# Kernel tuning notes

Measured on AMD Instinct MI355X. Metric: run time of the kernel, lower is better.

Reference implementation:

```python
import jax, jax.numpy as jnp
import numpy as np

N = 100000          # nodes
E = 3200000         # edges (avg degree 32)
F_IN = 128
HID = [128, 256, 128, 64, 32]
EPS = 1e-5


def setup_inputs() -> dict:
    key = jax.random.key(0)
    ks = jax.random.split(key, 64)
    inp = {}
    inp["x"] = jax.random.normal(ks[0], (N, F_IN), dtype=jnp.float32)
    inp["edge_index"] = jax.random.randint(ks[1], (2, E), 0, N, dtype=jnp.int64)
    dims = [F_IN] + HID
    k = 2
    for i in range(len(HID)):
        fan_in = dims[i]
        inp[f"W{i}"] = jax.random.normal(ks[k], (dims[i], dims[i + 1]), dtype=jnp.float32) / np.sqrt(fan_in); k += 1
        inp[f"b{i}"] = jnp.zeros((dims[i + 1],), dtype=jnp.float32)
        inp[f"g{i}"] = jnp.ones((dims[i + 1],), dtype=jnp.float32)
        inp[f"be{i}"] = jnp.zeros((dims[i + 1],), dtype=jnp.float32)
    inp["fc_w"] = jax.random.normal(ks[k], (HID[-1], 1), dtype=jnp.float32) / np.sqrt(HID[-1])
    inp["fc_b"] = jnp.zeros((1,), dtype=jnp.float32)
    return inp


def _gcn_forward(x, edge_index, Ws, bs, gs, bes, fc_w, fc_b):
    src, dst = edge_index[0], edge_index[1]
    # symmetric-normalized adjacency with self-loops (PyG GCNConv default,
    # edge_weight=None -> all-ones). deg = in-degree + 1 (self-loop).
    deg = jax.ops.segment_sum(jnp.ones((E,), x.dtype), dst, num_segments=N) + 1.0
    dis = jax.lax.rsqrt(deg)                 # deg^{-1/2}
    di = 1.0 / deg                           # self-loop norm deg^{-1}
    norm = (dis[src] * dis[dst])[:, None]    # [E,1]
    for W, b, g, be in zip(Ws, bs, gs, bes):
        h = x @ W                                                        # [N,d']
        x = jax.ops.segment_sum(norm * h[src], dst, num_segments=N)
        x = x + di[:, None] * h + b                                      # conv out
        mu = jnp.mean(x, axis=0)
        var = jnp.mean(jnp.square(x - mu), axis=0)
        x = (x - mu) * jax.lax.rsqrt(var + EPS) * g + be                 # BatchNorm1d
        x = jax.nn.relu(x)                                               # dropout = eval identity
    edge_emb = x[src] * x[dst]                                           # [E, 32]
    return jax.nn.sigmoid(edge_emb @ fc_w + fc_b)                        # [E, 1]


def reference(x, edge_index, W0, b0, g0, be0, W1, b1, g1, be1, W2, b2, g2, be2,
              W3, b3, g3, be3, W4, b4, g4, be4, fc_w, fc_b):
    Ws = [W0, W1, W2, W3, W4]
    bs = [b0, b1, b2, b3, b4]
    gs = [g0, g1, g2, g3, g4]
    bes = [be0, be1, be2, be3, be4]
    return _gcn_forward(x, edge_index, Ws, bs, gs, bes, fc_w, fc_b)
```

## Files before the change

### kernel.cpp

```cpp
#include <hip/hip_runtime.h>
#include <hip/hip_fp16.h>
#include <cstddef>

#define NN 100000
#define EE 3200000
#define EPSB 1e-5f
#define NB 391
#define BCAP 10240
#define BNBLK 512

typedef _Float16 half8 __attribute__((ext_vector_type(8)));
typedef float floatx4 __attribute__((ext_vector_type(4)));


__global__ __launch_bounds__(256) void k_bscat(const int* __restrict__ src,
                                               const int* __restrict__ dst,
                                               int* __restrict__ bcur,
                                               unsigned* __restrict__ barr) {
    __shared__ int hist[NB];
    __shared__ int base[NB];
    int tid = threadIdx.x;
    for (int b = tid; b < NB; b += 256) hist[b] = 0;
    __syncthreads();
    int e0 = blockIdx.x * 4096;
    int d[16], s[16];
    #pragma unroll
    for (int j = 0; j < 16; j++) {
        int e = e0 + j * 256 + tid;
        if (e < EE) {
            d[j] = dst[e];
            s[j] = src[e];
            atomicAdd(&hist[d[j] >> 8], 1);
        } else d[j] = -1;
    }
    __syncthreads();
    for (int b = tid; b < NB; b += 256) {
        int c = hist[b];
        base[b] = (c > 0) ? atomicAdd(&bcur[b], c) : 0;
        hist[b] = 0;
    }
    __syncthreads();
    #pragma unroll
    for (int j = 0; j < 16; j++) {
        if (d[j] >= 0) {
            int b = d[j] >> 8;
            int r = atomicAdd(&hist[b], 1);
            barr[(size_t)b * BCAP + base[b] + r] =
                (unsigned)s[j] | ((unsigned)(d[j] & 255) << 17);
        }
    }
}

__global__ __launch_bounds__(1024) void k_bdeg(const int* __restrict__ bcur,
                                               const unsigned* __restrict__ barr,
                                               int* __restrict__ degcnt,
                                               float* __restrict__ dis) {
    __shared__ int h[256];
    int b = blockIdx.x;
    if (threadIdx.x < 256) h[threadIdx.x] = 0;
    __syncthreads();
    int cnt = bcur[b];
    const unsigned* p = barr + (size_t)b * BCAP;
    for (int t = threadIdx.x; t < cnt; t += 1024)
        atomicAdd(&h[(p[t] >> 17) & 255], 1);
    __syncthreads();
    if (threadIdx.x < 256) {
        int node = (b << 8) + threadIdx.x;
        if (node < NN) {
            int dg = h[threadIdx.x];
            degcnt[node] = dg;
            dis[node] = rsqrtf((float)dg + 1.0f);
        }
    }
}

__global__ __launch_bounds__(1024) void k_place(const int* __restrict__ bcur,
                                                const unsigned* __restrict__ barr,
                                                const int* __restrict__ rowptr,
                                                int* __restrict__ col) {
    __shared__ int cur[256];
    int b = blockIdx.x;
    if (threadIdx.x < 256) {
        int node = (b << 8) + threadIdx.x;
        cur[threadIdx.x] = (node < NN) ? rowptr[node] : 0;
    }
    __syncthreads();
    int cnt = bcur[b];
    const unsigned* p = barr + (size_t)b * BCAP;
    for (int t = threadIdx.x; t < cnt; t += 1024) {
        unsigned e = p[t];
        int pos = atomicAdd(&cur[(e >> 17) & 255], 1);
        col[pos] = (int)(e & 0x1FFFFu);
    }
}

__global__ void k_scan_block(const int* __restrict__ in, int* __restrict__ out,
                             int* __restrict__ blksum, int n) {
    __shared__ int s[1024];
    int i = blockIdx.x * 1024 + threadIdx.x;
    int v = (i < n) ? in[i] : 0;
    s[threadIdx.x] = v;
    __syncthreads();
    for (int off = 1; off < 1024; off <<= 1) {
        int t = (threadIdx.x >= off) ? s[threadIdx.x - off] : 0;
        __syncthreads();
        s[threadIdx.x] += t;
        __syncthreads();
    }
    if (i < n) out[i] = s[threadIdx.x] - v;
    if (threadIdx.x == 1023) blksum[blockIdx.x] = s[1023];
}

__global__ void k_scan_top(int* __restrict__ blksum, int nb) {
    if (threadIdx.x == 0) {
        int acc = 0;
        for (int b = 0; b < nb; b++) { int v = blksum[b]; blksum[b] = acc; acc += v; }
    }
}

__global__ void k_scan_add(int* __restrict__ out, const int* __restrict__ blksum, int n) {
    int i = blockIdx.x * 1024 + threadIdx.x;
    if (i < n) out[i] += blksum[blockIdx.x];
}


__global__ void k_f2h(const float4* __restrict__ in, uint2* __restrict__ out, int n4) {
    int t = blockIdx.x * blockDim.x + threadIdx.x;
    if (t >= n4) return;
    float4 v = in[t];
    union { __half2 h; unsigned u; } a, b;
    a.h = __floats2half2_rn(v.x, v.y);
    b.h = __floats2half2_rn(v.z, v.w);
    out[t] = make_uint2(a.u, b.u);
}

__global__ void k_wpack_all(const float* __restrict__ W0, const float* __restrict__ W1,
                            const float* __restrict__ W2, const float* __restrict__ W3,
                            const float* __restrict__ W4, __half* __restrict__ Wp) {
    const int offs[6] = {0, 16384, 49152, 81920, 90112, 92160};
    const int Ks[5] = {128, 128, 256, 128, 64};
    const int Ns[5] = {128, 256, 128, 64, 32};
    const float* Ws[5] = {W0, W1, W2, W3, W4};
    int t = blockIdx.x * blockDim.x + threadIdx.x;
    if (t >= 92160) return;
    int l = 0;
    while (t >= offs[l + 1]) l++;
    int local = t - offs[l];
    int N = Ns[l], K = Ks[l];
    int k = local / N, n = local - k * N;
    Wp[(size_t)offs[l] + (size_t)n * K + k] = __float2half(Ws[l][local]);
}


template<int NT, bool OUT16, bool ABN>
__global__ __launch_bounds__(256) void k_mgemm(const void* __restrict__ Av,
                                               const __half* __restrict__ Wp,
                                               void* __restrict__ Cv,
                                               int M, int K, int N,
                                               const float* __restrict__ dis,
                                               const float* __restrict__ bias,
                                               const float* __restrict__ AB) {
    constexpr int TN = NT * 16;
    __shared__ __half Ash[128][40];
    __shared__ __half Bsh[TN][40];
    int tid  = threadIdx.x;
    int wave = tid >> 6;
    int lane = tid & 63;
    int quad = lane >> 4;
    int l16  = lane & 15;
    int bm = blockIdx.x * 128;
    int bn = blockIdx.y * TN;

    floatx4 acc[2][NT];
    #pragma unroll
    for (int mt = 0; mt < 2; mt++)
        #pragma unroll
        for (int nt = 0; nt < NT; nt++)
            acc[mt][nt] = (floatx4){0.f, 0.f, 0.f, 0.f};

    for (int k0 = 0; k0 < K; k0 += 32) {
        #pragma unroll
        for (int it = 0; it < 2; it++) {
            int u = tid + it * 256;
            int row = u >> 2, seg = u & 3;
            int grow = bm + row;
            if (ABN) {
                const float* Af = (const float*)Av;
                int f0 = k0 + seg * 8;
                uint4 o = make_uint4(0, 0, 0, 0);
                if (grow < M) {
                    float4 x0 = *(const float4*)&Af[(size_t)grow * K + f0];
                    float4 x1 = *(const float4*)&Af[(size_t)grow * K + f0 + 4];
                    float4 a0 = *(const float4*)&AB[f0];
                    float4 a1 = *(const float4*)&AB[f0 + 4];
                    float4 c0 = *(const float4*)&AB[K + f0];
                    float4 c1 = *(const float4*)&AB[K + f0 + 4];
                    float h0 = fmaxf(x0.x * a0.x + c0.x, 0.f);
                    float h1 = fmaxf(x0.y * a0.y + c0.y, 0.f);
                    float h2 = fmaxf(x0.z * a0.z + c0.z, 0.f);
                    float h3 = fmaxf(x0.w * a0.w + c0.w, 0.f);
                    float h4 = fmaxf(x1.x * a1.x + c1.x, 0.f);
                    float h5 = fmaxf(x1.y * a1.y + c1.y, 0.f);
                    float h6 = fmaxf(x1.z * a1.z + c1.z, 0.f);
                    float h7 = fmaxf(x1.w * a1.w + c1.w, 0.f);
                    union { __half2 h; unsigned u; } p0, p1, p2, p3;
                    p0.h = __floats2half2_rn(h0, h1);
                    p1.h = __floats2half2_rn(h2, h3);
                    p2.h = __floats2half2_rn(h4, h5);
                    p3.h = __floats2half2_rn(h6, h7);
                    o = make_uint4(p0.u, p1.u, p2.u, p3.u);
                }
                *(uint4*)&Ash[row][seg * 8] = o;
            } else {
                const __half* A = (const __half*)Av;
                uint4 v = make_uint4(0, 0, 0, 0);
                if (grow < M) v = *(const uint4*)&A[(size_t)grow * K + k0 + seg * 8];
                *(uint4*)&Ash[row][seg * 8] = v;
            }
        }
        if (tid < TN * 4) {
            int n = tid >> 2, seg = tid & 3;
            uint4 v = *(const uint4*)&Wp[(size_t)(bn + n) * K + k0 + seg * 8];
            *(uint4*)&Bsh[n][seg * 8] = v;
        }
        __syncthreads();
        half8 a[2], b[NT];
        #pragma unroll
        for (int mt = 0; mt < 2; mt++)
            a[mt] = *(const half8*)&Ash[wave * 32 + mt * 16 + l16][quad * 8];
        #pragma unroll
        for (int nt = 0; nt < NT; nt++)
            b[nt] = *(const half8*)&Bsh[nt * 16 + l16][quad * 8];
        #pragma unroll
        for (int mt = 0; mt < 2; mt++)
            #pragma unroll
            for (int nt = 0; nt < NT; nt++)
                acc[mt][nt] = __builtin_amdgcn_mfma_f32_16x16x32_f16(
                    a[mt], b[nt], acc[mt][nt], 0, 0, 0);
        __syncthreads();
    }

    #pragma unroll
    for (int mt = 0; mt < 2; mt++) {
        #pragma unroll
        for (int r = 0; r < 4; r++) {
            int grow = bm + wave * 32 + mt * 16 + quad * 4 + r;
            if (grow >= M) continue;
            if (OUT16) {
                float ds = dis[grow];
                __half* C = (__half*)Cv;
                #pragma unroll
                for (int nt = 0; nt < NT; nt++) {
                    int gcol = bn + nt * 16 + l16;
                    C[(size_t)grow * N + gcol] = __float2half(ds * acc[mt][nt][r]);
                }
            } else {
                float* C = (float*)Cv;
                #pragma unroll
                for (int nt = 0; nt < NT; nt++) {
                    int gcol = bn + nt * 16 + l16;
                    C[(size_t)grow * N + gcol] = acc[mt][nt][r] + bias[gcol];
                }
            }
        }
    }
}

__global__ void k_nscale(const float* __restrict__ X, const float* __restrict__ AB,
                         const float* __restrict__ dis, uint4* __restrict__ out) {
    int t = blockIdx.x * blockDim.x + threadIdx.x;
    if (t >= NN * 16) return;
    int row = t >> 4;
    int f0 = (t & 15) * 8;
    float ds = dis[row];
    float4 x0 = *(const float4*)&X[(size_t)row * 128 + f0];
    float4 x1 = *(const float4*)&X[(size_t)row * 128 + f0 + 4];
    float4 a0 = *(const float4*)&AB[f0];
    float4 a1 = *(const float4*)&AB[f0 + 4];
    float4 c0 = *(const float4*)&AB[128 + f0];
    float4 c1 = *(const float4*)&AB[128 + f0 + 4];
    float h0 = ds * fmaxf(x0.x * a0.x + c0.x, 0.f);
    float h1 = ds * fmaxf(x0.y * a0.y + c0.y, 0.f);
    float h2 = ds * fmaxf(x0.z * a0.z + c0.z, 0.f);
    float h3 = ds * fmaxf(x0.w * a0.w + c0.w, 0.f);
    float h4 = ds * fmaxf(x1.x * a1.x + c1.x, 0.f);
    float h5 = ds * fmaxf(x1.y * a1.y + c1.y, 0.f);
    float h6 = ds * fmaxf(x1.z * a1.z + c1.z, 0.f);
    float h7 = ds * fmaxf(x1.w * a1.w + c1.w, 0.f);
    union { __half2 h; unsigned u; } p0, p1, p2, p3;
    p0.h = __floats2half2_rn(h0, h1);
    p1.h = __floats2half2_rn(h2, h3);
    p2.h = __floats2half2_rn(h4, h5);
    p3.h = __floats2half2_rn(h6, h7);
    out[t] = make_uint4(p0.u, p1.u, p2.u, p3.u);
}


__device__ __forceinline__ void acc_row(float* acc, const uint4& r) {
    const __half2* hp = (const __half2*)&r;
    #pragma unroll
    for (int k = 0; k < 4; k++) {
        float2 f2 = __half22float2(hp[k]);
        acc[2 * k]     += f2.x;
        acc[2 * k + 1] += f2.y;
    }
}

template<int TPN, bool OUT16>
__global__ __launch_bounds__(256) void k_agg_h(const uint4* __restrict__ Hs,
                                               void* __restrict__ outv,
                                               const int* __restrict__ rowptr,
                                               const int* __restrict__ degcnt,
                                               const int* __restrict__ colv,
                                               const float* __restrict__ dis,
                                               const float* __restrict__ bias) {
    constexpr int G = 256 / TPN;
    int g    = threadIdx.x / TPN;
    int lane = threadIdx.x % TPN;
    int i = blockIdx.x * G + g;
    if (i >= NN) return;
    int beg = rowptr[i];
    int cnt = degcnt[i];
    const uint4* base = Hs + lane;
    float acc[8] = {};
    int e = 0;
    for (; e + 8 <= cnt; e += 8) {
        int c[8];
        #pragma unroll
        for (int j = 0; j < 8; j++) c[j] = colv[beg + e + j];
        uint4 r[8];
        #pragma unroll
        for (int j = 0; j < 8; j++) r[j] = base[(size_t)c[j] * TPN];
        #pragma unroll
        for (int j = 0; j < 8; j++) acc_row(acc, r[j]);
    }
    for (; e < cnt; e++) {
        uint4 r = base[(size_t)colv[beg + e] * TPN];
        acc_row(acc, r);
    }
    uint4 rs = base[(size_t)i * TPN];
    acc_row(acc, rs);
    float ds = dis[i];
    float o[8];
    #pragma unroll
    for (int k = 0; k < 8; k++) o[k] = ds * acc[k];
    if (OUT16) {
        uint4 ov;
        __half2* op = (__half2*)&ov;
        #pragma unroll
        for (int k = 0; k < 4; k++) op[k] = __floats2half2_rn(o[2 * k], o[2 * k + 1]);
        ((uint4*)outv)[(size_t)i * TPN + lane] = ov;
    } else {
        float4 b0 = ((const float4*)bias)[lane * 2];
        float4 b1 = ((const float4*)bias)[lane * 2 + 1];
        o[0] += b0.x; o[1] += b0.y; o[2] += b0.z; o[3] += b0.w;
        o[4] += b1.x; o[5] += b1.y; o[6] += b1.z; o[7] += b1.w;
        float4* out = (float4*)outv;
        size_t ob = (size_t)i * (2 * TPN) + lane * 2;
        out[ob]     = make_float4(o[0], o[1], o[2], o[3]);
        out[ob + 1] = make_float4(o[4], o[5], o[6], o[7]);
    }
}


template<int D>
__global__ __launch_bounds__(256) void k_bnpart(const float4* __restrict__ X4,
                                                float* __restrict__ partial) {
    constexpr int Q   = D / 4;
    constexpr int RPI = 256 / Q;
    int tq = threadIdx.x % Q;
    int rg = threadIdx.x / Q;
    int chunk = (NN + BNBLK - 1) / BNBLK;
    int r0 = blockIdx.x * chunk;
    int r1 = r0 + chunk; if (r1 > NN) r1 = NN;
    float4 s  = {0.f, 0.f, 0.f, 0.f};
    float4 s2 = {0.f, 0.f, 0.f, 0.f};
    for (int r = r0 + rg; r < r1; r += RPI) {
        float4 v = X4[(size_t)r * Q + tq];
        s.x += v.x; s.y += v.y; s.z += v.z; s.w += v.w;
        s2.x += v.x * v.x; s2.y += v.y * v.y; s2.z += v.z * v.z; s2.w += v.w * v.w;
    }
    __shared__ float4 ls[256], ls2[256];
    ls[threadIdx.x] = s; ls2[threadIdx.x] = s2;
    __syncthreads();
    if (threadIdx.x < Q) {
        float4 a = ls[threadIdx.x], b = ls2[threadIdx.x];
        #pragma unroll
        for (int g = 1; g < RPI; g++) {
            float4 u = ls[g * Q + threadIdx.x], w = ls2[g * Q + threadIdx.x];
            a.x += u.x; a.y += u.y; a.z += u.z; a.w += u.w;
            b.x += w.x; b.y += w.y; b.z += w.z; b.w += w.w;
        }
        *(float4*)&partial[(size_t)blockIdx.x * 2 * D + threadIdx.x * 4]     = a;
        *(float4*)&partial[(size_t)blockIdx.x * 2 * D + D + threadIdx.x * 4] = b;
    }
}

template<int D>
__global__ __launch_bounds__(1024) void k_bnfin2(const float* __restrict__ partial,
                                                 const float* __restrict__ g,
                                                 const float* __restrict__ be,
                                                 float* __restrict__ AB) {
    constexpr int G = 1024 / D;
    int f  = threadIdx.x % D;
    int gr = threadIdx.x / D;
    float sum = 0.f, sq = 0.f;
    for (int b = gr; b < BNBLK; b += G) {
        sum += partial[(size_t)b * 2 * D + f];
        sq  += partial[(size_t)b * 2 * D + D + f];
    }
    __shared__ float ls[1024], ls2[1024];
    ls[threadIdx.x] = sum; ls2[threadIdx.x] = sq;
    __syncthreads();
    if (threadIdx.x < D) {
        float a = ls[threadIdx.x], b = ls2[threadIdx.x];
        for (int k = 1; k < G; k++) {
            a += ls[k * D + threadIdx.x];
            b += ls2[k * D + threadIdx.x];
        }
        float mu  = a / (float)NN;
        float var = b / (float)NN - mu * mu;
        var = fmaxf(var, 0.f);
        float inv = rsqrtf(var + EPSB);
        float sc = g[threadIdx.x] * inv;
        AB[threadIdx.x]     = sc;
        AB[D + threadIdx.x] = be[threadIdx.x] - mu * sc;
    }
}

__global__ void k_norm16(const float4* __restrict__ X, const float* __restrict__ AB,
                         uint2* __restrict__ Y, int d, int total4) {
    int t = blockIdx.x * blockDim.x + threadIdx.x;
    if (t >= total4) return;
    int f0 = (t * 4) & (d - 1);
    float4 v = X[t];
    float a0 = AB[f0],     a1 = AB[f0 + 1], a2 = AB[f0 + 2], a3 = AB[f0 + 3];
    float c0 = AB[d + f0], c1 = AB[d + f0 + 1], c2 = AB[d + f0 + 2], c3 = AB[d + f0 + 3];
    float o0 = fmaxf(v.x * a0 + c0, 0.f);
    float o1 = fmaxf(v.y * a1 + c1, 0.f);
    float o2 = fmaxf(v.z * a2 + c2, 0.f);
    float o3 = fmaxf(v.w * a3 + c3, 0.f);
    union { __half2 h; unsigned u; } p, q;
    p.h = __floats2half2_rn(o0, o1);
    q.h = __floats2half2_rn(o2, o3);
    Y[t] = make_uint2(p.u, q.u);
}


__global__ __launch_bounds__(256) void k_edge16(const uint4* __restrict__ X,
                                                const int* __restrict__ src,
                                                const int* __restrict__ dst,
                                                const float* __restrict__ fcw,
                                                const float* __restrict__ fcb,
                                                float* __restrict__ out) {
    int lane = threadIdx.x & 3;
    size_t t = (size_t)blockIdx.x * 256 + threadIdx.x;
    int eid = (int)(t >> 2);
    if (eid >= EE) return;
    int s = src[eid], d = dst[eid];
    uint4 av = X[(size_t)s * 4 + lane];
    uint4 bv = X[(size_t)d * 4 + lane];
    const __half2* ap = (const __half2*)&av;
    const __half2* bp2 = (const __half2*)&bv;
    float v = 0.f;
    #pragma unroll
    for (int k = 0; k < 4; k++) {
        float2 fa = __half22float2(ap[k]);
        float2 fb = __half22float2(bp2[k]);
        float w0 = fcw[lane * 8 + 2 * k];
        float w1 = fcw[lane * 8 + 2 * k + 1];
        v += fa.x * fb.x * w0 + fa.y * fb.y * w1;
    }
    v += __shfl_xor(v, 1, 4);
    v += __shfl_xor(v, 2, 4);
    if (lane == 0) out[eid] = 1.f / (1.f + expf(-(v + fcb[0])));
}


extern "C" void kernel_launch(void* const* d_in, const int* in_sizes, int n_in,
                              void* d_out, int out_size, void* d_ws, size_t ws_size,
                              hipStream_t stream) {
    const float* x0 = (const float*)d_in[0];
    const int* ei   = (const int*)d_in[1];
    const int* srcv = ei;
    const int* dstv = ei + EE;
    const float *W[5], *bp[5], *gp[5], *bep[5];
    int idx = 2;
    for (int l = 0; l < 5; l++) {
        W[l]   = (const float*)d_in[idx++];
        bp[l]  = (const float*)d_in[idx++];
        gp[l]  = (const float*)d_in[idx++];
        bep[l] = (const float*)d_in[idx++];
    }
    const float* fcw = (const float*)d_in[22];
    const float* fcb = (const float*)d_in[23];

    char* ws = (char*)d_ws;
    size_t off = 0;
    auto alloc = [&](size_t bytes) -> void* {
        void* p = ws + off;
        off = (off + bytes + 255) & ~(size_t)255;
        return p;
    };
    float*    bufA    = (float*)   alloc((size_t)NN * 256 * 4);
    __half*   act16   = (__half*)  alloc((size_t)NN * 256 * 2);
    __half*   x16     = (__half*)  alloc((size_t)NN * 128 * 2);
    __half*   Hh      = (__half*)  alloc((size_t)NN * 128 * 2);
    unsigned* barr    = (unsigned*)alloc((size_t)NB * BCAP * 4);
    int*      colv    = (int*)     alloc((size_t)EE * 4);
    int*      rowptr  = (int*)     alloc((size_t)NN * 4);
    int*      degcnt  = (int*)     alloc((size_t)NN * 4);
    float*    dis     = (float*)   alloc((size_t)NN * 4);
    int*      bcur    = (int*)     alloc((size_t)NB * 4);
    int*      scnblk  = (int*)     alloc(4096);
    float*    bnpart  = (float*)   alloc((size_t)BNBLK * 512 * 4);
    float*    bnAB    = (float*)   alloc(512 * 4);
    __half*   Wp      = (__half*)  alloc((size_t)92160 * 2);
    const int woff[5] = {0, 16384, 49152, 81920, 90112};

    hipMemsetAsync(bcur, 0, (size_t)NB * 4, stream);
    k_bscat<<<(EE + 4095) / 4096, 256, 0, stream>>>(srcv, dstv, bcur, barr);
    k_bdeg<<<NB, 1024, 0, stream>>>(bcur, barr, degcnt, dis);
    int nScanBlk = (NN + 1023) / 1024;
    k_scan_block<<<nScanBlk, 1024, 0, stream>>>(degcnt, rowptr, scnblk, NN);
    k_scan_top<<<1, 64, 0, stream>>>(scnblk, nScanBlk);
    k_scan_add<<<nScanBlk, 1024, 0, stream>>>(rowptr, scnblk, NN);
    k_place<<<NB, 1024, 0, stream>>>(bcur, barr, rowptr, colv);

    k_f2h<<<(NN * 128 / 4 + 255) / 256, 256, 0, stream>>>(
        (const float4*)x0, (uint2*)x16, NN * 128 / 4);
    k_wpack_all<<<(92160 + 255) / 256, 256, 0, stream>>>(W[0], W[1], W[2], W[3], W[4], Wp);

    int gx = (NN + 127) / 128;

    {
        dim3 grid(gx, 128 / 64);
        k_mgemm<4, true, false><<<grid, 256, 0, stream>>>(x16, Wp + woff[0], Hh, NN, 128, 128, dis, nullptr, nullptr);
        k_agg_h<16, false><<<(NN + 15) / 16, 256, 0, stream>>>(
            (const uint4*)Hh, bufA, rowptr, degcnt, colv, dis, bp[0]);
        k_bnpart<128><<<BNBLK, 256, 0, stream>>>((const float4*)bufA, bnpart);
        k_bnfin2<128><<<1, 1024, 0, stream>>>(bnpart, gp[0], bep[0], bnAB);
        k_nscale<<<(NN * 16 + 255) / 256, 256, 0, stream>>>(bufA, bnAB, dis, (uint4*)Hh);
    }
    {
        k_agg_h<16, true><<<(NN + 15) / 16, 256, 0, stream>>>(
            (const uint4*)Hh, act16, rowptr, degcnt, colv, dis, nullptr);
        dim3 grid(gx, 256 / 64);
        k_mgemm<4, false, false><<<grid, 256, 0, stream>>>(act16, Wp + woff[1], bufA, NN, 128, 256, nullptr, bp[1], nullptr);
        k_bnpart<256><<<BNBLK, 256, 0, stream>>>((const float4*)bufA, bnpart);
        k_bnfin2<256><<<1, 1024, 0, stream>>>(bnpart, gp[1], bep[1], bnAB);
    }
    {
        dim3 grid(gx, 128 / 64);
        k_mgemm<4, true, true><<<grid, 256, 0, stream>>>(bufA, Wp + woff[2], Hh, NN, 256, 128, dis, nullptr, bnAB);
        k_agg_h<16, false><<<(NN + 15) / 16, 256, 0, stream>>>(
            (const uint4*)Hh, bufA, rowptr, degcnt, colv, dis, bp[2]);
        k_bnpart<128><<<BNBLK, 256, 0, stream>>>((const float4*)bufA, bnpart);
        k_bnfin2<128><<<1, 1024, 0, stream>>>(bnpart, gp[2], bep[2], bnAB);
    }
    {
        dim3 grid(gx, 64 / 64);
        k_mgemm<4, true, true><<<grid, 256, 0, stream>>>(bufA, Wp + woff[3], Hh, NN, 128, 64, dis, nullptr, bnAB);
        k_agg_h<8, false><<<(NN + 31) / 32, 256, 0, stream>>>(
            (const uint4*)Hh, bufA, rowptr, degcnt, colv, dis, bp[3]);
        k_bnpart<64><<<BNBLK, 256, 0, stream>>>((const float4*)bufA, bnpart);
        k_bnfin2<64><<<1, 1024, 0, stream>>>(bnpart, gp[3], bep[3], bnAB);
    }
    {
        dim3 grid(gx, 1);
        k_mgemm<2, true, true><<<grid, 256, 0, stream>>>(bufA, Wp + woff[4], Hh, NN, 64, 32, dis, nullptr, bnAB);
        k_agg_h<4, false><<<(NN + 63) / 64, 256, 0, stream>>>(
            (const uint4*)Hh, bufA, rowptr, degcnt, colv, dis, bp[4]);
        k_bnpart<32><<<BNBLK, 256, 0, stream>>>((const float4*)bufA, bnpart);
        k_bnfin2<32><<<1, 1024, 0, stream>>>(bnpart, gp[4], bep[4], bnAB);
        int total4 = NN * 32 / 4;
        k_norm16<<<(total4 + 255) / 256, 256, 0, stream>>>(
            (const float4*)bufA, bnAB, (uint2*)act16, 32, total4);
    }

    size_t edgeThreads = (size_t)EE * 4;
    k_edge16<<<(unsigned)((edgeThreads + 255) / 256), 256, 0, stream>>>(
        (const uint4*)act16, srcv, dstv, fcw, fcb, (float*)d_out);
}
```

Before: 1.004 ms.

## Quantize gathered features to int8 with per-group scales for first two aggregations

Adds int8 quantization of the node feature rows gathered in the first two layers' aggregations. Layer 0 uses signed values with a zero point and one scale per 8 features; layer 1 uses unsigned values with one scale per 16 features after ReLU. This halves the bytes per gathered row and reuses the edge-bucket buffer for storage. It also deepens the unroll of the fp16 gather loop to 16, with a 4-wide tail. The cost is extra quantize passes, scale-array reads and lower numerical precision.

```diff
diff --git a/kernel.cpp b/kernel.cpp
--- a/kernel.cpp
+++ b/kernel.cpp
@@ -266,8 +266,38 @@
     }
 }
 
-__global__ void k_nscale(const float* __restrict__ X, const float* __restrict__ AB,
-                         const float* __restrict__ dis, uint4* __restrict__ out) {
+
+__global__ __launch_bounds__(256) void k_q8p8(const uint4* __restrict__ H,
+                                              uint2* __restrict__ q8,
+                                              float* __restrict__ scq, int total) {
+    int t = blockIdx.x * 256 + threadIdx.x;
+    if (t >= total) return;
+    uint4 v = H[t];
+    const __half2* hp = (const __half2*)&v;
+    float h[8];
+    #pragma unroll
+    for (int k = 0; k < 4; k++) {
+        float2 f = __half22float2(hp[k]);
+        h[2 * k] = f.x; h[2 * k + 1] = f.y;
+    }
+    float m = fabsf(h[0]);
+    #pragma unroll
+    for (int k = 1; k < 8; k++) m = fmaxf(m, fabsf(h[k]));
+    float inv = m > 0.f ? 127.f / m : 0.f;
+    unsigned b[8];
+    #pragma unroll
+    for (int k = 0; k < 8; k++) {
+        float f = fminf(fmaxf(h[k] * inv, -127.f), 127.f);
+        b[k] = (unsigned)(f + 128.5f);
+    }
+    q8[t] = make_uint2(b[0] | (b[1] << 8) | (b[2] << 16) | (b[3] << 24),
+                       b[4] | (b[5] << 8) | (b[6] << 16) | (b[7] << 24));
+    scq[t] = m * (1.f / 127.f);
+}
+
+__global__ void k_nscale_q8(const float* __restrict__ X, const float* __restrict__ AB,
+                            const float* __restrict__ dis, uint2* __restrict__ q8,
+                            float* __restrict__ scq) {
     int t = blockIdx.x * blockDim.x + threadIdx.x;
     if (t >= NN * 16) return;
     int row = t >> 4;
@@ -279,22 +309,172 @@
     float4 a1 = *(const float4*)&AB[f0 + 4];
     float4 c0 = *(const float4*)&AB[128 + f0];
     float4 c1 = *(const float4*)&AB[128 + f0 + 4];
-    float h0 = ds * fmaxf(x0.x * a0.x + c0.x, 0.f);
-    float h1 = ds * fmaxf(x0.y * a0.y + c0.y, 0.f);
-    float h2 = ds * fmaxf(x0.z * a0.z + c0.z, 0.f);
-    float h3 = ds * fmaxf(x0.w * a0.w + c0.w, 0.f);
-    float h4 = ds * fmaxf(x1.x * a1.x + c1.x, 0.f);
-    float h5 = ds * fmaxf(x1.y * a1.y + c1.y, 0.f);
-    float h6 = ds * fmaxf(x1.z * a1.z + c1.z, 0.f);
-    float h7 = ds * fmaxf(x1.w * a1.w + c1.w, 0.f);
-    union { __half2 h; unsigned u; } p0, p1, p2, p3;
-    p0.h = __floats2half2_rn(h0, h1);
-    p1.h = __floats2half2_rn(h2, h3);
-    p2.h = __floats2half2_rn(h4, h5);
-    p3.h = __floats2half2_rn(h6, h7);
-    out[t] = make_uint4(p0.u, p1.u, p2.u, p3.u);
-}
-
+    float h[8];
+    h[0] = ds * fmaxf(x0.x * a0.x + c0.x, 0.f);
+    h[1] = ds * fmaxf(x0.y * a0.y + c0.y, 0.f);
+    h[2] = ds * fmaxf(x0.z * a0.z + c0.z, 0.f);
+    h[3] = ds * fmaxf(x0.w * a0.w + c0.w, 0.f);
+    h[4] = ds * fmaxf(x1.x * a1.x + c1.x, 0.f);
+    h[5] = ds * fmaxf(x1.y * a1.y + c1.y, 0.f);
+    h[6] = ds * fmaxf(x1.z * a1.z + c1.z, 0.f);
+    h[7] = ds * fmaxf(x1.w * a1.w + c1.w, 0.f);
+    float m = h[0];
+    #pragma unroll
+    for (int k = 1; k < 8; k++) m = fmaxf(m, h[k]);
+    m = fmaxf(m, __shfl_xor(m, 1));
+    float inv = m > 0.f ? 255.f / m : 0.f;
+    unsigned b[8];
+    #pragma unroll
+    for (int k = 0; k < 8; k++)
+        b[k] = (unsigned)(fminf(h[k] * inv, 255.f) + 0.5f);
+    q8[t] = make_uint2(b[0] | (b[1] << 8) | (b[2] << 16) | (b[3] << 24),
+                       b[4] | (b[5] << 8) | (b[6] << 16) | (b[7] << 24));
+    if ((t & 1) == 0) scq[t >> 1] = m * (1.f / 255.f);
+}
+
+
+__device__ __forceinline__ void acc_q8s2(float* acc, const uint4& r,
+                                         const float2& s, float& c0, float& c1) {
+    const unsigned* w = (const unsigned*)&r;
+    c0 += s.x; c1 += s.y;
+    #pragma unroll
+    for (int q = 0; q < 4; q++) {
+        unsigned v = w[q];
+        float sq = (q < 2) ? s.x : s.y;
+        acc[4 * q + 0] = fmaf(sq, (float)(v & 0xffu), acc[4 * q + 0]);
+        acc[4 * q + 1] = fmaf(sq, (float)((v >> 8) & 0xffu), acc[4 * q + 1]);
+        acc[4 * q + 2] = fmaf(sq, (float)((v >> 16) & 0xffu), acc[4 * q + 2]);
+        acc[4 * q + 3] = fmaf(sq, (float)(v >> 24), acc[4 * q + 3]);
+    }
+}
+
+template<int TPN>
+__global__ __launch_bounds__(256) void k_agg_q8s(const uint4* __restrict__ Q,
+                                                 const float* __restrict__ sc,
+                                                 float* __restrict__ outf,
+                                                 const int* __restrict__ rowptr,
+                                                 const int* __restrict__ degcnt,
+                                                 const int* __restrict__ colv,
+                                                 const float* __restrict__ dis,
+                                                 const float* __restrict__ bias) {
+    constexpr int G = 256 / TPN;
+    int g    = threadIdx.x / TPN;
+    int lane = threadIdx.x % TPN;
+    int i = blockIdx.x * G + g;
+    if (i >= NN) return;
+    int beg = rowptr[i];
+    int cnt = degcnt[i];
+    const uint4*  base = Q + lane;
+    const float2* scb  = (const float2*)sc + lane;
+    float acc[16] = {};
+    float c0 = 0.f, c1 = 0.f;
+    int e = 0;
+    for (; e + 8 <= cnt; e += 8) {
+        int c[8];
+        #pragma unroll
+        for (int j = 0; j < 8; j++) c[j] = colv[beg + e + j];
+        uint4 r[8];
+        float2 s[8];
+        #pragma unroll
+        for (int j = 0; j < 8; j++) {
+            r[j] = base[(size_t)c[j] * TPN];
+            s[j] = scb[(size_t)c[j] * TPN];
+        }
+        #pragma unroll
+        for (int j = 0; j < 8; j++) acc_q8s2(acc, r[j], s[j], c0, c1);
+    }
+    for (; e < cnt; e++) {
+        int c = colv[beg + e];
+        uint4 r = base[(size_t)c * TPN];
+        acc_q8s2(acc, r, scb[(size_t)c * TPN], c0, c1);
+    }
+    uint4 rs = base[(size_t)i * TPN];
+    acc_q8s2(acc, rs, scb[(size_t)i * TPN], c0, c1);
+    float ds = dis[i];
+    float zp0 = 128.f * c0, zp1 = 128.f * c1;
+    float o[16];
+    #pragma unroll
+    for (int k = 0; k < 16; k++) o[k] = ds * (acc[k] - (k < 8 ? zp0 : zp1));
+    float4* out = (float4*)outf;
+    const float4* bi = (const float4*)bias;
+    size_t ob = (size_t)i * (4 * TPN) + lane * 4;
+    #pragma unroll
+    for (int j = 0; j < 4; j++) {
+        float4 b = bi[lane * 4 + j];
+        out[ob + j] = make_float4(o[4 * j] + b.x, o[4 * j + 1] + b.y,
+                                  o[4 * j + 2] + b.z, o[4 * j + 3] + b.w);
+    }
+}
+
+__device__ __forceinline__ void acc_q8u(float* acc, const uint4& r, float s) {
+    const unsigned* w = (const unsigned*)&r;
+    #pragma unroll
+    for (int q = 0; q < 4; q++) {
+        unsigned v = w[q];
+        acc[4 * q + 0] = fmaf(s, (float)(v & 0xffu), acc[4 * q + 0]);
+        acc[4 * q + 1] = fmaf(s, (float)((v >> 8) & 0xffu), acc[4 * q + 1]);
+        acc[4 * q + 2] = fmaf(s, (float)((v >> 16) & 0xffu), acc[4 * q + 2]);
+        acc[4 * q + 3] = fmaf(s, (float)(v >> 24), acc[4 * q + 3]);
+    }
+}
+
+template<int TPN>
+__global__ __launch_bounds__(256) void k_agg_q8u(const uint4* __restrict__ Q,
+                                                 const float* __restrict__ sc,
+                                                 __half* __restrict__ out16,
+                                                 const int* __restrict__ rowptr,
+                                                 const int* __restrict__ degcnt,
+                                                 const int* __restrict__ colv,
+                                                 const float* __restrict__ dis) {
+    constexpr int G = 256 / TPN;
+    int g    = threadIdx.x / TPN;
+    int lane = threadIdx.x % TPN;
+    int i = blockIdx.x * G + g;
+    if (i >= NN) return;
+    int beg = rowptr[i];
+    int cnt = degcnt[i];
+    const uint4* base = Q + lane;
+    const float* scb  = sc + lane;
+    float acc[16] = {};
+    int e = 0;
+    for (; e + 8 <= cnt; e += 8) {
+        int c[8];
+        #pragma unroll
+        for (int j = 0; j < 8; j++) c[j] = colv[beg + e + j];
+        uint4 r[8];
+        float s[8];
+        #pragma unroll
+        for (int j = 0; j < 8; j++) {
+            r[j] = base[(size_t)c[j] * TPN];
+            s[j] = scb[(size_t)c[j] * TPN];
+        }
+        #pragma unroll
+        for (int j = 0; j < 8; j++) acc_q8u(acc, r[j], s[j]);
+    }
+    for (; e < cnt; e++) {
+        int c = colv[beg + e];
+        uint4 r = base[(size_t)c * TPN];
+        acc_q8u(acc, r, scb[(size_t)c * TPN]);
+    }
+    uint4 rs = base[(size_t)i * TPN];
+    acc_q8u(acc, rs, scb[(size_t)i * TPN]);
+    float ds = dis[i];
+    float o[16];
+    #pragma unroll
+    for (int k = 0; k < 16; k++) o[k] = ds * acc[k];
+    uint4 ov0, ov1;
+    __half2* p0 = (__half2*)&ov0;
+    __half2* p1 = (__half2*)&ov1;
+    #pragma unroll
+    for (int k = 0; k < 4; k++) {
+        p0[k] = __floats2half2_rn(o[2 * k], o[2 * k + 1]);
+        p1[k] = __floats2half2_rn(o[8 + 2 * k], o[9 + 2 * k]);
+    }
+    uint4* out = (uint4*)out16;
+    size_t ob = (size_t)i * (2 * TPN) + lane * 2;
+    out[ob]     = ov0;
+    out[ob + 1] = ov1;
+}
 
 __device__ __forceinline__ void acc_row(float* acc, const uint4& r) {
     const __half2* hp = (const __half2*)&r;
@@ -324,15 +504,25 @@
     const uint4* base = Hs + lane;
     float acc[8] = {};
     int e = 0;
-    for (; e + 8 <= cnt; e += 8) {
-        int c[8];
-        #pragma unroll
-        for (int j = 0; j < 8; j++) c[j] = colv[beg + e + j];
-        uint4 r[8];
-        #pragma unroll
-        for (int j = 0; j < 8; j++) r[j] = base[(size_t)c[j] * TPN];
-        #pragma unroll
-        for (int j = 0; j < 8; j++) acc_row(acc, r[j]);
+    for (; e + 16 <= cnt; e += 16) {
+        int c[16];
+        #pragma unroll
+        for (int j = 0; j < 16; j++) c[j] = colv[beg + e + j];
+        uint4 r[16];
+        #pragma unroll
+        for (int j = 0; j < 16; j++) r[j] = base[(size_t)c[j] * TPN];
+        #pragma unroll
+        for (int j = 0; j < 16; j++) acc_row(acc, r[j]);
+    }
+    for (; e + 4 <= cnt; e += 4) {
+        int c[4];
+        #pragma unroll
+        for (int j = 0; j < 4; j++) c[j] = colv[beg + e + j];
+        uint4 r[4];
+        #pragma unroll
+        for (int j = 0; j < 4; j++) r[j] = base[(size_t)c[j] * TPN];
+        #pragma unroll
+        for (int j = 0; j < 4; j++) acc_row(acc, r[j]);
     }
     for (; e < cnt; e++) {
         uint4 r = base[(size_t)colv[beg + e] * TPN];
@@ -516,7 +706,10 @@
     float*    bnpart  = (float*)   alloc((size_t)BNBLK * 512 * 4);
     float*    bnAB    = (float*)   alloc(512 * 4);
     __half*   Wp      = (__half*)  alloc((size_t)92160 * 2);
+    float*    scq     = (float*)   alloc((size_t)NN * 16 * 4);
     const int woff[5] = {0, 16384, 49152, 81920, 90112};
+
+    unsigned char* q8 = (unsigned char*)barr;
 
     hipMemsetAsync(bcur, 0, (size_t)NB * 4, stream);
     k_bscat<<<(EE + 4095) / 4096, 256, 0, stream>>>(srcv, dstv, bcur, barr);
@@ -536,15 +729,16 @@
     {
         dim3 grid(gx, 128 / 64);
         k_mgemm<4, true, false><<<grid, 256, 0, stream>>>(x16, Wp + woff[0], Hh, NN, 128, 128, dis, nullptr, nullptr);
-        k_agg_h<16, false><<<(NN + 15) / 16, 256, 0, stream>>>(
-            (const uint4*)Hh, bufA, rowptr, degcnt, colv, dis, bp[0]);
+        k_q8p8<<<NN * 16 / 256, 256, 0, stream>>>((const uint4*)Hh, (uint2*)q8, scq, NN * 16);
+        k_agg_q8s<8><<<(NN + 31) / 32, 256, 0, stream>>>(
+            (const uint4*)q8, scq, bufA, rowptr, degcnt, colv, dis, bp[0]);
         k_bnpart<128><<<BNBLK, 256, 0, stream>>>((const float4*)bufA, bnpart);
         k_bnfin2<128><<<1, 1024, 0, stream>>>(bnpart, gp[0], bep[0], bnAB);
-        k_nscale<<<(NN * 16 + 255) / 256, 256, 0, stream>>>(bufA, bnAB, dis, (uint4*)Hh);
+        k_nscale_q8<<<(NN * 16 + 255) / 256, 256, 0, stream>>>(bufA, bnAB, dis, (uint2*)q8, scq);
     }
     {
-        k_agg_h<16, true><<<(NN + 15) / 16, 256, 0, stream>>>(
-            (const uint4*)Hh, act16, rowptr, degcnt, colv, dis, nullptr);
+        k_agg_q8u<8><<<(NN + 31) / 32, 256, 0, stream>>>(
+            (const uint4*)q8, scq, act16, rowptr, degcnt, colv, dis);
         dim3 grid(gx, 256 / 64);
         k_mgemm<4, false, false><<<grid, 256, 0, stream>>>(act16, Wp + woff[1], bufA, NN, 128, 256, nullptr, bp[1], nullptr);
         k_bnpart<256><<<BNBLK, 256, 0, stream>>>((const float4*)bufA, bnpart);
```

Result: faster. 984.5 us (-2.0%).

## Store fp16 features in column-sliced layout for per-slice gather aggregation

Applied to the files above, without the earlier changes.

The GEMM and node-scale kernels now write half-precision features in a sliced layout: each 16-feature slice is stored contiguously across all nodes. Aggregation is split into one block per slice, with two threads per node, so each block's gather touches a smaller working set that may stay resident in cache. The cost is more blocks and reading colv/rowptr once per slice, and each gathered row becomes only 32 bytes, which may lower memory efficiency.

```diff
diff --git a/kernel.cpp b/kernel.cpp
--- a/kernel.cpp
+++ b/kernel.cpp
@@ -8,6 +8,7 @@
 #define NB 391
 #define BCAP 10240
 #define BNBLK 512
+#define NBLK128 782
 
 typedef _Float16 half8 __attribute__((ext_vector_type(8)));
 typedef float floatx4 __attribute__((ext_vector_type(4)));
@@ -152,7 +153,7 @@
 }
 
 
-template<int NT, bool OUT16, bool ABN>
+template<int NT, bool OUT16, bool ABN, bool SLC>
 __global__ __launch_bounds__(256) void k_mgemm(const void* __restrict__ Av,
                                                const __half* __restrict__ Wp,
                                                void* __restrict__ Cv,
@@ -252,7 +253,10 @@
                 #pragma unroll
                 for (int nt = 0; nt < NT; nt++) {
                     int gcol = bn + nt * 16 + l16;
-                    C[(size_t)grow * N + gcol] = __float2half(ds * acc[mt][nt][r]);
+                    size_t addr = SLC
+                        ? (size_t)(gcol >> 4) * ((size_t)NN * 16) + (size_t)grow * 16 + l16
+                        : (size_t)grow * N + gcol;
+                    C[addr] = __float2half(ds * acc[mt][nt][r]);
                 }
             } else {
                 float* C = (float*)Cv;
@@ -266,12 +270,13 @@
     }
 }
 
-__global__ void k_nscale(const float* __restrict__ X, const float* __restrict__ AB,
-                         const float* __restrict__ dis, uint4* __restrict__ out) {
+__global__ void k_nscale_sl(const float* __restrict__ X, const float* __restrict__ AB,
+                            const float* __restrict__ dis, uint4* __restrict__ out) {
     int t = blockIdx.x * blockDim.x + threadIdx.x;
     if (t >= NN * 16) return;
     int row = t >> 4;
-    int f0 = (t & 15) * 8;
+    int sub = t & 15;
+    int f0 = sub * 8;
     float ds = dis[row];
     float4 x0 = *(const float4*)&X[(size_t)row * 128 + f0];
     float4 x1 = *(const float4*)&X[(size_t)row * 128 + f0 + 4];
@@ -292,7 +297,8 @@
     p1.h = __floats2half2_rn(h2, h3);
     p2.h = __floats2half2_rn(h4, h5);
     p3.h = __floats2half2_rn(h6, h7);
-    out[t] = make_uint4(p0.u, p1.u, p2.u, p3.u);
+    out[(size_t)(sub >> 1) * (NN * 2) + (size_t)row * 2 + (sub & 1)] =
+        make_uint4(p0.u, p1.u, p2.u, p3.u);
 }
 
 
@@ -306,22 +312,23 @@
     }
 }
 
-template<int TPN, bool OUT16>
-__global__ __launch_bounds__(256) void k_agg_h(const uint4* __restrict__ Hs,
-                                               void* __restrict__ outv,
-                                               const int* __restrict__ rowptr,
-                                               const int* __restrict__ degcnt,
-                                               const int* __restrict__ colv,
-                                               const float* __restrict__ dis,
-                                               const float* __restrict__ bias) {
-    constexpr int G = 256 / TPN;
-    int g    = threadIdx.x / TPN;
-    int lane = threadIdx.x % TPN;
-    int i = blockIdx.x * G + g;
+template<int NS, bool OUT16>
+__global__ __launch_bounds__(256) void k_agg_sl(const uint4* __restrict__ Hs,
+                                                void* __restrict__ outv,
+                                                const int* __restrict__ rowptr,
+                                                const int* __restrict__ degcnt,
+                                                const int* __restrict__ colv,
+                                                const float* __restrict__ dis,
+                                                const float* __restrict__ bias) {
+    int slice = blockIdx.x % NS;
+    int nblk  = blockIdx.x / NS;
+    int g     = threadIdx.x >> 1;
+    int lane  = threadIdx.x & 1;
+    int i = nblk * 128 + g;
     if (i >= NN) return;
     int beg = rowptr[i];
     int cnt = degcnt[i];
-    const uint4* base = Hs + lane;
+    const uint4* base = Hs + (size_t)slice * (NN * 2) + lane;
     float acc[8] = {};
     int e = 0;
     for (; e + 8 <= cnt; e += 8) {
@@ -330,16 +337,13 @@
         for (int j = 0; j < 8; j++) c[j] = colv[beg + e + j];
         uint4 r[8];
         #pragma unroll
-        for (int j = 0; j < 8; j++) r[j] = base[(size_t)c[j] * TPN];
+        for (int j = 0; j < 8; j++) r[j] = base[(size_t)c[j] * 2];
         #pragma unroll
         for (int j = 0; j < 8; j++) acc_row(acc, r[j]);
     }
-    for (; e < cnt; e++) {
-        uint4 r = base[(size_t)colv[beg + e] * TPN];
-        acc_row(acc, r);
-    }
-    uint4 rs = base[(size_t)i * TPN];
-    acc_row(acc, rs);
+    for (; e < cnt; e++)
+        acc_row(acc, base[(size_t)colv[beg + e] * 2]);
+    acc_row(acc, base[(size_t)i * 2]);
     float ds = dis[i];
     float o[8];
     #pragma unroll
@@ -349,16 +353,15 @@
         __half2* op = (__half2*)&ov;
         #pragma unroll
         for (int k = 0; k < 4; k++) op[k] = __floats2half2_rn(o[2 * k], o[2 * k + 1]);
-        ((uint4*)outv)[(size_t)i * TPN + lane] = ov;
+        ((uint4*)outv)[(size_t)i * (NS * 2) + slice * 2 + lane] = ov;
     } else {
-        float4 b0 = ((const float4*)bias)[lane * 2];
-        float4 b1 = ((const float4*)bias)[lane * 2 + 1];
-        o[0] += b0.x; o[1] += b0.y; o[2] += b0.z; o[3] += b0.w;
-        o[4] += b1.x; o[5] += b1.y; o[6] += b1.z; o[7] += b1.w;
+        const float4* bi = (const float4*)bias;
+        float4 b0 = bi[slice * 4 + lane * 2];
+        float4 b1 = bi[slice * 4 + lane * 2 + 1];
         float4* out = (float4*)outv;
-        size_t ob = (size_t)i * (2 * TPN) + lane * 2;
-        out[ob]     = make_float4(o[0], o[1], o[2], o[3]);
-        out[ob + 1] = make_float4(o[4], o[5], o[6], o[7]);
+        size_t ob = (size_t)i * (NS * 4) + slice * 4 + lane * 2;
+        out[ob]     = make_float4(o[0] + b0.x, o[1] + b0.y, o[2] + b0.z, o[3] + b0.w);
+        out[ob + 1] = make_float4(o[4] + b1.x, o[5] + b1.y, o[6] + b1.z, o[7] + b1.w);
     }
 }
 
@@ -535,41 +538,46 @@
 
     {
         dim3 grid(gx, 128 / 64);
-        k_mgemm<4, true, false><<<grid, 256, 0, stream>>>(x16, Wp + woff[0], Hh, NN, 128, 128, dis, nullptr, nullptr);
-        k_agg_h<16, false><<<(NN + 15) / 16, 256, 0, stream>>>(
+        k_mgemm<4, true, false, true><<<grid, 256, 0, stream>>>(
+            x16, Wp + woff[0], Hh, NN, 128, 128, dis, nullptr, nullptr);
+        k_agg_sl<8, false><<<NBLK128 * 8, 256, 0, stream>>>(
             (const uint4*)Hh, bufA, rowptr, degcnt, colv, dis, bp[0]);
         k_bnpart<128><<<BNBLK, 256, 0, stream>>>((const float4*)bufA, bnpart);
         k_bnfin2<128><<<1, 1024, 0, stream>>>(bnpart, gp[0], bep[0], bnAB);
-        k_nscale<<<(NN * 16 + 255) / 256, 256, 0, stream>>>(bufA, bnAB, dis, (uint4*)Hh);
+        k_nscale_sl<<<(NN * 16 + 255) / 256, 256, 0, stream>>>(bufA, bnAB, dis, (uint4*)Hh);
     }
     {
-        k_agg_h<16, true><<<(NN + 15) / 16, 256, 0, stream>>>(
+        k_agg_sl<8, true><<<NBLK128 * 8, 256, 0, stream>>>(
             (const uint4*)Hh, act16, rowptr, degcnt, colv, dis, nullptr);
         dim3 grid(gx, 256 / 64);
-        k_mgemm<4, false, false><<<grid, 256, 0, stream>>>(act16, Wp + woff[1], bufA, NN, 128, 256, nullptr, bp[1], nullptr);
+        k_mgemm<4, false, false, false><<<grid, 256, 0, stream>>>(
+            act16, Wp + woff[1], bufA, NN, 128, 256, nullptr, bp[1], nullptr);
         k_bnpart<256><<<BNBLK, 256, 0, stream>>>((const float4*)bufA, bnpart);
         k_bnfin2<256><<<1, 1024, 0, stream>>>(bnpart, gp[1], bep[1], bnAB);
     }
     {
         dim3 grid(gx, 128 / 64);
-        k_mgemm<4, true, true><<<grid, 256, 0, stream>>>(bufA, Wp + woff[2], Hh, NN, 256, 128, dis, nullptr, bnAB);
-        k_agg_h<16, false><<<(NN + 15) / 16, 256, 0, stream>>>(
+        k_mgemm<4, true, true, true><<<grid, 256, 0, stream>>>(
+            bufA, Wp + woff[2], Hh, NN, 256, 128, dis, nullptr, bnAB);
+        k_agg_sl<8, false><<<NBLK128 * 8, 256, 0, stream>>>(
             (const uint4*)Hh, bufA, rowptr, degcnt, colv, dis, bp[2]);
         k_bnpart<128><<<BNBLK, 256, 0, stream>>>((const float4*)bufA, bnpart);
         k_bnfin2<128><<<1, 1024, 0, stream>>>(bnpart, gp[2], bep[2], bnAB);
     }
     {
         dim3 grid(gx, 64 / 64);
-        k_mgemm<4, true, true><<<grid, 256, 0, stream>>>(bufA, Wp + woff[3], Hh, NN, 128, 64, dis, nullptr, bnAB);
-        k_agg_h<8, false><<<(NN + 31) / 32, 256, 0, stream>>>(
+        k_mgemm<4, true, true, true><<<grid, 256, 0, stream>>>(
+            bufA, Wp + woff[3], Hh, NN, 128, 64, dis, nullptr, bnAB);
+        k_agg_sl<4, false><<<NBLK128 * 4, 256, 0, stream>>>(
             (const uint4*)Hh, bufA, rowptr, degcnt, colv, dis, bp[3]);
         k_bnpart<64><<<BNBLK, 256, 0, stream>>>((const float4*)bufA, bnpart);
         k_bnfin2<64><<<1, 1024, 0, stream>>>(bnpart, gp[3], bep[3], bnAB);
     }
     {
         dim3 grid(gx, 1);
-        k_mgemm<2, true, true><<<grid, 256, 0, stream>>>(bufA, Wp + woff[4], Hh, NN, 64, 32, dis, nullptr, bnAB);
-        k_agg_h<4, false><<<(NN + 63) / 64, 256, 0, stream>>>(
+        k_mgemm<2, true, true, true><<<grid, 256, 0, stream>>>(
+            bufA, Wp + woff[4], Hh, NN, 64, 32, dis, nullptr, bnAB);
+        k_agg_sl<2, false><<<NBLK128 * 2, 256, 0, stream>>>(
             (const uint4*)Hh, bufA, rowptr, degcnt, colv, dis, bp[4]);
         k_bnpart<32><<<BNBLK, 256, 0, stream>>>((const float4*)bufA, bnpart);
         k_bnfin2<32><<<1, 1024, 0, stream>>>(bnpart, gp[4], bep[4], bnAB);
```

New measurement: 1.264 ms. 1.26x slower.

## Slice 128-wide features into column slabs and aggregate slab-by-slab per XCC

Applied to the files above, without the earlier changes.

The 128-wide fp16 node features are now written in a column-sliced layout: 8 slabs of 16 features for every node. A new persistent aggregation kernel walks those slabs. Each workgroup starts on a slab chosen by its XCC id and pulls 128-node chunks from an atomic work queue, so each gather touches a 3.2 MB slab that can stay resident in that XCC's L2 instead of hitting random rows of the full matrix. Outputs and column index loads use nontemporal operations. The cost is that colv and rowptr are re-read once per slab, 8 times in all, and the design leans on the hardware XCC register and queue scheduling.

```diff
diff --git a/kernel.cpp b/kernel.cpp
--- a/kernel.cpp
+++ b/kernel.cpp
@@ -8,9 +8,21 @@
 #define NB 391
 #define BCAP 10240
 #define BNBLK 512
+#define NBLK128 782
 
 typedef _Float16 half8 __attribute__((ext_vector_type(8)));
 typedef float floatx4 __attribute__((ext_vector_type(4)));
+typedef float f32x4v __attribute__((ext_vector_type(4)));
+typedef unsigned u32x4v __attribute__((ext_vector_type(4)));
+
+__device__ __forceinline__ void nt_store_f4(const float4& v, float4* p) {
+    f32x4v t = {v.x, v.y, v.z, v.w};
+    __builtin_nontemporal_store(t, (f32x4v*)p);
+}
+__device__ __forceinline__ void nt_store_u4(const uint4& v, uint4* p) {
+    u32x4v t = {v.x, v.y, v.z, v.w};
+    __builtin_nontemporal_store(t, (u32x4v*)p);
+}
 
 
 __global__ __launch_bounds__(256) void k_bscat(const int* __restrict__ src,
@@ -152,7 +164,7 @@
 }
 
 
-template<int NT, bool OUT16, bool ABN>
+template<int NT, bool OUT16, bool ABN, bool SLC>
 __global__ __launch_bounds__(256) void k_mgemm(const void* __restrict__ Av,
                                                const __half* __restrict__ Wp,
                                                void* __restrict__ Cv,
@@ -252,7 +264,10 @@
                 #pragma unroll
                 for (int nt = 0; nt < NT; nt++) {
                     int gcol = bn + nt * 16 + l16;
-                    C[(size_t)grow * N + gcol] = __float2half(ds * acc[mt][nt][r]);
+                    size_t addr = SLC
+                        ? (size_t)(gcol >> 4) * ((size_t)NN * 16) + (size_t)grow * 16 + l16
+                        : (size_t)grow * N + gcol;
+                    C[addr] = __float2half(ds * acc[mt][nt][r]);
                 }
             } else {
                 float* C = (float*)Cv;
@@ -266,12 +281,13 @@
     }
 }
 
-__global__ void k_nscale(const float* __restrict__ X, const float* __restrict__ AB,
-                         const float* __restrict__ dis, uint4* __restrict__ out) {
+__global__ void k_nscale_sl(const float* __restrict__ X, const float* __restrict__ AB,
+                            const float* __restrict__ dis, uint4* __restrict__ out) {
     int t = blockIdx.x * blockDim.x + threadIdx.x;
     if (t >= NN * 16) return;
     int row = t >> 4;
-    int f0 = (t & 15) * 8;
+    int sub = t & 15;
+    int f0 = sub * 8;
     float ds = dis[row];
     float4 x0 = *(const float4*)&X[(size_t)row * 128 + f0];
     float4 x1 = *(const float4*)&X[(size_t)row * 128 + f0 + 4];
@@ -292,9 +308,16 @@
     p1.h = __floats2half2_rn(h2, h3);
     p2.h = __floats2half2_rn(h4, h5);
     p3.h = __floats2half2_rn(h6, h7);
-    out[t] = make_uint4(p0.u, p1.u, p2.u, p3.u);
-}
-
+    out[(size_t)(sub >> 1) * (NN * 2) + (size_t)row * 2 + (sub & 1)] =
+        make_uint4(p0.u, p1.u, p2.u, p3.u);
+}
+
+
+__device__ __forceinline__ int xcc_id() {
+    unsigned v;
+    asm("s_getreg_b32 %0, hwreg(HW_REG_XCC_ID)" : "=s"(v));
+    return (int)v;
+}
 
 __device__ __forceinline__ void acc_row(float* acc, const uint4& r) {
     const __half2* hp = (const __half2*)&r;
@@ -303,6 +326,76 @@
         float2 f2 = __half22float2(hp[k]);
         acc[2 * k]     += f2.x;
         acc[2 * k + 1] += f2.y;
+    }
+}
+
+template<bool OUT16>
+__global__ __launch_bounds__(256) void k_agg_x(const uint4* __restrict__ Hs,
+                                               void* __restrict__ outv,
+                                               const int* __restrict__ rowptr,
+                                               const int* __restrict__ degcnt,
+                                               const int* __restrict__ colv,
+                                               const float* __restrict__ dis,
+                                               const float* __restrict__ bias,
+                                               int* __restrict__ wq) {
+    __shared__ int sblk;
+    int xcc  = xcc_id() & 7;
+    int g    = threadIdx.x >> 1;
+    int lane = threadIdx.x & 1;
+    for (int sv = 0; sv < 8; sv++) {
+        int s = (xcc + sv) & 7;
+        const uint4* base = Hs + (size_t)s * (NN * 2) + lane;
+        for (;;) {
+            __syncthreads();
+            if (threadIdx.x == 0) sblk = atomicAdd(&wq[s], 1);
+            __syncthreads();
+            int nb = sblk;
+            if (nb >= NBLK128) break;
+            int i = nb * 128 + g;
+            if (i >= NN) continue;
+            int beg = rowptr[i];
+            int cnt = degcnt[i];
+            float acc[8] = {};
+            int e = 0;
+            for (; e + 8 <= cnt; e += 8) {
+                int c[8];
+                #pragma unroll
+                for (int j = 0; j < 8; j++)
+                    c[j] = __builtin_nontemporal_load(&colv[beg + e + j]);
+                uint4 r[8];
+                #pragma unroll
+                for (int j = 0; j < 8; j++) r[j] = base[(size_t)c[j] * 2];
+                #pragma unroll
+                for (int j = 0; j < 8; j++) acc_row(acc, r[j]);
+            }
+            for (; e < cnt; e++) {
+                int c = __builtin_nontemporal_load(&colv[beg + e]);
+                acc_row(acc, base[(size_t)c * 2]);
+            }
+            acc_row(acc, base[(size_t)i * 2]);
+            float ds = dis[i];
+            float o[8];
+            #pragma unroll
+            for (int k = 0; k < 8; k++) o[k] = ds * acc[k];
+            if (OUT16) {
+                uint4 ov;
+                __half2* op = (__half2*)&ov;
+                #pragma unroll
+                for (int k = 0; k < 4; k++)
+                    op[k] = __floats2half2_rn(o[2 * k], o[2 * k + 1]);
+                nt_store_u4(ov, &((uint4*)outv)[(size_t)i * 16 + s * 2 + lane]);
+            } else {
+                const float4* bi = (const float4*)bias;
+                float4 b0 = bi[s * 4 + lane * 2];
+                float4 b1 = bi[s * 4 + lane * 2 + 1];
+                float4* out = (float4*)outv;
+                size_t ob = (size_t)i * 32 + s * 4 + lane * 2;
+                nt_store_f4(make_float4(o[0] + b0.x, o[1] + b0.y,
+                                        o[2] + b0.z, o[3] + b0.w), &out[ob]);
+                nt_store_f4(make_float4(o[4] + b1.x, o[5] + b1.y,
+                                        o[6] + b1.z, o[7] + b1.w), &out[ob + 1]);
+            }
+        }
     }
 }
 
@@ -516,9 +609,11 @@
     float*    bnpart  = (float*)   alloc((size_t)BNBLK * 512 * 4);
     float*    bnAB    = (float*)   alloc(512 * 4);
     __half*   Wp      = (__half*)  alloc((size_t)92160 * 2);
+    int*      wq      = (int*)     alloc(3 * 8 * 4);
     const int woff[5] = {0, 16384, 49152, 81920, 90112};
 
     hipMemsetAsync(bcur, 0, (size_t)NB * 4, stream);
+    hipMemsetAsync(wq, 0, 3 * 8 * 4, stream);
     k_bscat<<<(EE + 4095) / 4096, 256, 0, stream>>>(srcv, dstv, bcur, barr);
     k_bdeg<<<NB, 1024, 0, stream>>>(bcur, barr, degcnt, dis);
     int nScanBlk = (NN + 1023) / 1024;
@@ -535,32 +630,36 @@
 
     {
         dim3 grid(gx, 128 / 64);
-        k_mgemm<4, true, false><<<grid, 256, 0, stream>>>(x16, Wp + woff[0], Hh, NN, 128, 128, dis, nullptr, nullptr);
-        k_agg_h<16, false><<<(NN + 15) / 16, 256, 0, stream>>>(
-            (const uint4*)Hh, bufA, rowptr, degcnt, colv, dis, bp[0]);
+        k_mgemm<4, true, false, true><<<grid, 256, 0, stream>>>(
+            x16, Wp + woff[0], Hh, NN, 128, 128, dis, nullptr, nullptr);
+        k_agg_x<false><<<2048, 256, 0, stream>>>(
+            (const uint4*)Hh, bufA, rowptr, degcnt, colv, dis, bp[0], wq);
         k_bnpart<128><<<BNBLK, 256, 0, stream>>>((const float4*)bufA, bnpart);
         k_bnfin2<128><<<1, 1024, 0, stream>>>(bnpart, gp[0], bep[0], bnAB);
-        k_nscale<<<(NN * 16 + 255) / 256, 256, 0, stream>>>(bufA, bnAB, dis, (uint4*)Hh);
+        k_nscale_sl<<<(NN * 16 + 255) / 256, 256, 0, stream>>>(bufA, bnAB, dis, (uint4*)Hh);
     }
     {
-        k_agg_h<16, true><<<(NN + 15) / 16, 256, 0, stream>>>(
-            (const uint4*)Hh, act16, rowptr, degcnt, colv, dis, nullptr);
+        k_agg_x<true><<<2048, 256, 0, stream>>>(
+            (const uint4*)Hh, act16, rowptr, degcnt, colv, dis, nullptr, wq + 8);
         dim3 grid(gx, 256 / 64);
-        k_mgemm<4, false, false><<<grid, 256, 0, stream>>>(act16, Wp + woff[1], bufA, NN, 128, 256, nullptr, bp[1], nullptr);
+        k_mgemm<4, false, false, false><<<grid, 256, 0, stream>>>(
+            act16, Wp + woff[1], bufA, NN, 128, 256, nullptr, bp[1], nullptr);
         k_bnpart<256><<<BNBLK, 256, 0, stream>>>((const float4*)bufA, bnpart);
         k_bnfin2<256><<<1, 1024, 0, stream>>>(bnpart, gp[1], bep[1], bnAB);
     }
     {
         dim3 grid(gx, 128 / 64);
-        k_mgemm<4, true, true><<<grid, 256, 0, stream>>>(bufA, Wp + woff[2], Hh, NN, 256, 128, dis, nullptr, bnAB);
-        k_agg_h<16, false><<<(NN + 15) / 16, 256, 0, stream>>>(
-            (const uint4*)Hh, bufA, rowptr, degcnt, colv, dis, bp[2]);
+        k_mgemm<4, true, true, true><<<grid, 256, 0, stream>>>(
+            bufA, Wp + woff[2], Hh, NN, 256, 128, dis, nullptr, bnAB);
+        k_agg_x<false><<<2048, 256, 0, stream>>>(
+            (const uint4*)Hh, bufA, rowptr, degcnt, colv, dis, bp[2], wq + 16);
         k_bnpart<128><<<BNBLK, 256, 0, stream>>>((const float4*)bufA, bnpart);
         k_bnfin2<128><<<1, 1024, 0, stream>>>(bnpart, gp[2], bep[2], bnAB);
     }
     {
         dim3 grid(gx, 64 / 64);
-        k_mgemm<4, true, true><<<grid, 256, 0, stream>>>(bufA, Wp + woff[3], Hh, NN, 128, 64, dis, nullptr, bnAB);
+        k_mgemm<4, true, true, false><<<grid, 256, 0, stream>>>(
+            bufA, Wp + woff[3], Hh, NN, 128, 64, dis, nullptr, bnAB);
         k_agg_h<8, false><<<(NN + 31) / 32, 256, 0, stream>>>(
             (const uint4*)Hh, bufA, rowptr, degcnt, colv, dis, bp[3]);
         k_bnpart<64><<<BNBLK, 256, 0, stream>>>((const float4*)bufA, bnpart);
@@ -568,7 +667,8 @@
     }
     {
         dim3 grid(gx, 1);
-        k_mgemm<2, true, true><<<grid, 256, 0, stream>>>(bufA, Wp + woff[4], Hh, NN, 64, 32, dis, nullptr, bnAB);
+        k_mgemm<2, true, true, false><<<grid, 256, 0, stream>>>(
+            bufA, Wp + woff[4], Hh, NN, 64, 32, dis, nullptr, bnAB);
         k_agg_h<4, false><<<(NN + 63) / 64, 256, 0, stream>>>(
             (const uint4*)Hh, bufA, rowptr, degcnt, colv, dis, bp[4]);
         k_bnpart<32><<<BNBLK, 256, 0, stream>>>((const float4*)bufA, bnpart);
```

Result: slower. 1.933 ms (+92.4%).
